# Kernel optimization log

Measured on AMD Instinct MI355X. Metric: run time of the kernel, lower is better.

Reference implementation:

```python
import jax, jax.numpy as jnp
import numpy as np

EPS = 1e-6  # matches nn.CosineSimilarity(eps=1e-6) and the log-denominator eps


def setup_inputs() -> dict:
    key = jax.random.key(0)
    k1, k2 = jax.random.split(key)
    bs, d = 8192, 128
    f = jax.random.normal(k1, (bs, d), dtype=jnp.float32)
    noise = jax.random.normal(k2, (bs, d), dtype=jnp.float32)
    return {"f": f, "noise": noise}


def reference(f, noise):
    bs = f.shape[0]
    cat = jnp.concatenate([noise, f], axis=0)  # [2bs, d]
    # torch CosineSimilarity: x.y / max(||x||*||y||, eps)
    nf = jnp.linalg.norm(f, axis=1)    # [bs]
    nc = jnp.linalg.norm(cat, axis=1)  # [2bs]
    sims = (f @ cat.T) / jnp.maximum(nf[:, None] * nc[None, :], EPS)  # [bs, 2bs]
    m = jnp.exp(sims)
    idx = jnp.arange(bs)
    pos = m[idx, idx]                 # f[i] vs noise[i]
    self_sim = m[idx, idx + bs]       # f[i] vs f[i], excluded from negatives
    neg_sum = m.sum(axis=1) - pos - self_sim
    loss = -jnp.log(pos / (neg_sum + EPS))
    return loss.mean()
```

## Files before the change

### kernel.cpp

```cpp
#include <hip/hip_runtime.h>
#include <hip/hip_bf16.h>
#include <math.h>

#define BS 8192
#define D 128
#define NROWS 16384
#define COLS_PER_BLOCK 512
#define NCHUNK (COLS_PER_BLOCK / 16)
#define NSPLIT (NROWS / COLS_PER_BLOCK)
#define NPART NSPLIT

typedef int i32x4 __attribute__((ext_vector_type(4)));
typedef int i32x8 __attribute__((ext_vector_type(8)));
typedef float f32x4 __attribute__((ext_vector_type(4)));

#define LN2F 0.6931471805599453f
#define STORE_SCALE 19.217958569050494f
#define E8M0_M4 123
#define FMT_FP4 4

#if __has_builtin(__builtin_amdgcn_exp2f)
#define EXP2F(x) __builtin_amdgcn_exp2f(x)
#else
#define EXP2F(x) exp2f(x)
#endif


__global__ __launch_bounds__(256) void nrm_cvt(const float* __restrict__ f,
                                               const float* __restrict__ noise,
                                               char* __restrict__ catF,
                                               unsigned int* __restrict__ cnt) {
  if (blockIdx.x == 0 && threadIdx.x == 0) cnt[0] = 0;
  const int lane = threadIdx.x & 63;
  const int wv = threadIdx.x >> 6;
  const int row = blockIdx.x * 4 + wv;
  const float* src = (row < BS) ? (noise + (size_t)row * D) : (f + (size_t)(row - BS) * D);
  float2 v = ((const float2*)src)[lane];
  float ss = v.x * v.x + v.y * v.y;
#pragma unroll
  for (int m = 1; m <= 32; m <<= 1) ss += __shfl_xor(ss, m, 64);
  const float s = STORE_SCALE / sqrtf(ss);
  auto q4 = [](float x) {
    const float av = fabsf(x);
    int c = (av > 0.25f) + (av > 0.75f) + (av > 1.25f) + (av > 1.75f) +
            (av > 2.5f) + (av > 3.5f) + (av > 5.0f);
    return c | ((x < 0.f) ? 8 : 0);
  };
  const int b = q4(v.x * s) | (q4(v.y * s) << 4);
  const int b1 = __shfl_down(b, 1, 64);
  const int b2 = __shfl_down(b, 2, 64);
  const int b3 = __shfl_down(b, 3, 64);
  if ((lane & 3) == 0) {
    const unsigned word = (unsigned)b | ((unsigned)b1 << 8) |
                          ((unsigned)b2 << 16) | ((unsigned)b3 << 24);
    char* dst = catF + ((size_t)(row >> 4) << 10) + ((lane >> 4) << 8) +
                ((row & 15) << 4) + (lane & 15);
    *(unsigned*)dst = word;
  }
}

__device__ __forceinline__ i32x8 mk8(i32x4 v) {
  i32x8 r = {v[0], v[1], v[2], v[3], 0, 0, 0, 0};
  return r;
}

__global__ __launch_bounds__(256) void infonce_main(
    const char* __restrict__ catF,
    float* __restrict__ ws_neg, float* __restrict__ ws_pos) {
  const int tid = threadIdx.x;
  const int lane = tid & 63;
  const int w = tid >> 6;
  const int l15 = lane & 15, l4 = lane >> 4;
  const int nb = blockIdx.x, mb = blockIdx.y;
  const int growbase = mb * 256 + w * 64;
  const int col0 = nb * COLS_PER_BLOCK;
  const int lbase = l4 * 256 + l15 * 16;

  i32x8 a[4];
  {
    const char* ab = catF + ((size_t)((BS + growbase) >> 4) << 10) + lbase;
#pragma unroll
    for (int rf = 0; rf < 4; rf++) a[rf] = mk8(*(const i32x4*)(ab + rf * 1024));
  }

  f32x4 rs[4];
  const f32x4 z = {0.f, 0.f, 0.f, 0.f};
#pragma unroll
  for (int rf = 0; rf < 4; rf++) rs[rf] = z;

  const char* bl = catF + ((size_t)(col0 >> 4) << 10) + lbase;

  auto ld = [&](int c) { return mk8(*(const i32x4*)(bl + (size_t)c * 1024)); };

  auto domfma = [&](f32x4* acc, const i32x8& b) {
#pragma unroll
    for (int rf = 0; rf < 4; rf++)
      acc[rf] = __builtin_amdgcn_mfma_scale_f32_16x16x128_f8f6f4(
          a[rf], b, z, FMT_FP4, FMT_FP4, 0, E8M0_M4, 0, E8M0_M4);
  };

  auto epi = [&](const f32x4* acc, int c) {
    const int c0 = col0 + c * 16;
    const bool dPos = ((c0 & ~63) == growbase);
    const bool dSelf = (((c0 - BS) & ~63) == growbase);
    if (!dPos && !dSelf) {
#pragma unroll
      for (int rf = 0; rf < 4; rf++) {
        f32x4 e;
#pragma unroll
        for (int r = 0; r < 4; r++) e[r] = EXP2F(acc[rf][r]);
        rs[rf] += e;
      }
    } else {
#pragma unroll
      for (int rf = 0; rf < 4; rf++)
#pragma unroll
        for (int r = 0; r < 4; r++) {
          const int grow = growbase + rf * 16 + l4 * 4 + r;
          const int gcol = c0 + l15;
          const float v = acc[rf][r];
          const bool ex = dPos ? (gcol == grow) : (gcol == grow + BS);
          if (dPos && gcol == grow) ws_pos[grow] = v;
          rs[rf][r] += ex ? 0.f : EXP2F(v);
        }
    }
  };

  i32x8 bb[4];
  bb[0] = ld(0);
  bb[1] = ld(1);

  f32x4 accA[4], accB[4];
  domfma(accA, bb[0]);
  bb[2] = ld(2);
  domfma(accB, bb[1]);
  bb[3] = ld(3);

#pragma unroll
  for (int ph = 0; ph < 15; ++ph) {
    const int c = 2 * ph;
    __builtin_amdgcn_sched_barrier(0);
    epi(accA, c);
    if (c + 4 < NCHUNK) bb[(c + 4) & 3] = ld(c + 4);
    domfma(accA, bb[(c + 2) & 3]);
    __builtin_amdgcn_sched_barrier(0);
    epi(accB, c + 1);
    if (c + 5 < NCHUNK) bb[(c + 5) & 3] = ld(c + 5);
    domfma(accB, bb[(c + 3) & 3]);
  }
  __builtin_amdgcn_sched_barrier(0);
  epi(accA, NCHUNK - 2);
  epi(accB, NCHUNK - 1);

  float rowsum[16];
#pragma unroll
  for (int rf = 0; rf < 4; rf++)
#pragma unroll
    for (int r = 0; r < 4; r++) {
      float v = rs[rf][r];
      v += __shfl_xor(v, 1, 64);
      v += __shfl_xor(v, 2, 64);
      v += __shfl_xor(v, 4, 64);
      v += __shfl_xor(v, 8, 64);
      rowsum[rf * 4 + r] = v;
    }
  if (l15 == 0) {
    float* dst = ws_neg + (size_t)nb * BS + growbase;
#pragma unroll
    for (int rf = 0; rf < 4; rf++)
#pragma unroll
      for (int r = 0; r < 4; r++) dst[rf * 16 + l4 * 4 + r] = rowsum[rf * 4 + r];
  }
}

__global__ __launch_bounds__(256) void finalize(const float* __restrict__ ws_neg,
                                                const float* __restrict__ ws_pos,
                                                float* __restrict__ partial,
                                                unsigned int* __restrict__ cnt,
                                                float* __restrict__ out) {
  __shared__ float red[4];
  __shared__ int flag;
  const int tid = threadIdx.x;
  const int lane = tid & 63;
  const int w = tid >> 6;
  const int row = blockIdx.x * 256 + tid;
  float neg = 0.f;
#pragma unroll
  for (int p = 0; p < NPART; p++) neg += ws_neg[(size_t)p * BS + row];
  float local = logf(neg + 1e-6f) - ws_pos[row] * LN2F;
#pragma unroll
  for (int m = 1; m <= 32; m <<= 1) local += __shfl_xor(local, m, 64);
  if (lane == 0) red[w] = local;
  __syncthreads();
  if (tid == 0) {
    partial[blockIdx.x] = red[0] + red[1] + red[2] + red[3];
    __threadfence();
    flag = (atomicAdd(cnt, 1u) == (unsigned)(BS / 256 - 1));
  }
  __syncthreads();
  if (!flag) return;
  __threadfence();
  if (tid < 64) {
    float v = (tid < 32) ? partial[tid] : 0.f;
#pragma unroll
    for (int m = 1; m <= 32; m <<= 1) v += __shfl_xor(v, m, 64);
    if (tid == 0) out[0] = v * (1.f / BS);
  }
}

extern "C" void kernel_launch(void* const* d_in, const int* in_sizes, int n_in,
                              void* d_out, int out_size, void* d_ws, size_t ws_size,
                              hipStream_t stream) {
  const float* f = (const float*)d_in[0];
  const float* noise = (const float*)d_in[1];
  char* ws = (char*)d_ws;
  char* catF = ws;
  float* ws_pos = (float*)(ws + (size_t)NROWS * 64);
  float* ws_neg = ws_pos + BS;
  float* partial = ws_neg + (size_t)NPART * BS;
  unsigned int* cnt = (unsigned int*)(partial + 32);

  nrm_cvt<<<NROWS / 4, 256, 0, stream>>>(f, noise, catF, cnt);
  dim3 grid(NSPLIT, BS / 256);
  infonce_main<<<grid, 256, 0, stream>>>(catF, ws_neg, ws_pos);
  finalize<<<BS / 256, 256, 0, stream>>>(ws_neg, ws_pos, partial, cnt, (float*)d_out);
}
```

Before: 36.11 us.

## Exploit symmetry of f·fᵀ block to halve self-similarity MFMA and exp work

Splits the work into noise-column jobs and upper-triangular f×f tile jobs. Each off-diagonal f×f tile adds its exp values to both row sums and column partial sums, so the symmetric half is never computed. Diagonal tiles mask the lower triangle, which also drops the self-similarity term. The aim is to cut MFMA and exp work on the f×f half by about half. In exchange the kernel adds shared-memory column reductions, a triangular index mapping, and a heavier finalize pass that reads more partial buffers.

```diff
diff --git a/kernel.cpp b/kernel.cpp
--- a/kernel.cpp
+++ b/kernel.cpp
@@ -5,10 +5,9 @@
 #define BS 8192
 #define D 128
 #define NROWS 16384
-#define COLS_PER_BLOCK 512
-#define NCHUNK (COLS_PER_BLOCK / 16)
-#define NSPLIT (NROWS / COLS_PER_BLOCK)
-#define NPART NSPLIT
+#define NJOBS_N 512
+#define NJOBS_F 528
+#define NJOBS (NJOBS_N + NJOBS_F)
 
 typedef int i32x4 __attribute__((ext_vector_type(4)));
 typedef int i32x8 __attribute__((ext_vector_type(8)));
@@ -66,114 +65,212 @@
 
 __global__ __launch_bounds__(256) void infonce_main(
     const char* __restrict__ catF,
-    float* __restrict__ ws_neg, float* __restrict__ ws_pos) {
+    float* __restrict__ wsN, float* __restrict__ rowF,
+    float* __restrict__ colP, float* __restrict__ ws_pos) {
+  __shared__ float cls[4][256];
   const int tid = threadIdx.x;
   const int lane = tid & 63;
   const int w = tid >> 6;
   const int l15 = lane & 15, l4 = lane >> 4;
-  const int nb = blockIdx.x, mb = blockIdx.y;
-  const int growbase = mb * 256 + w * 64;
-  const int col0 = nb * COLS_PER_BLOCK;
+  const int jid = blockIdx.x;
+  const f32x4 z = {0.f, 0.f, 0.f, 0.f};
+
+  f32x4 rs[4];
+#pragma unroll
+  for (int rf = 0; rf < 4; rf++) rs[rf] = z;
   const int lbase = l4 * 256 + l15 * 16;
 
-  i32x8 a[4];
-  {
-    const char* ab = catF + ((size_t)((BS + growbase) >> 4) << 10) + lbase;
-#pragma unroll
-    for (int rf = 0; rf < 4; rf++) a[rf] = mk8(*(const i32x4*)(ab + rf * 1024));
+  if (jid < NJOBS_N) {
+    const int mb = jid >> 4, nb = jid & 15;
+    const int growbase = mb * 256 + w * 64;
+    const int col0 = nb * 512;
+
+    i32x8 a[4];
+    {
+      const char* ab = catF + ((size_t)((BS + growbase) >> 4) << 10) + lbase;
+#pragma unroll
+      for (int rf = 0; rf < 4; rf++) a[rf] = mk8(*(const i32x4*)(ab + rf * 1024));
+    }
+    const char* bl = catF + ((size_t)(col0 >> 4) << 10) + lbase;
+    auto ld = [&](int c) { return mk8(*(const i32x4*)(bl + (size_t)c * 1024)); };
+    auto domfma = [&](f32x4* acc, const i32x8& b) {
+#pragma unroll
+      for (int rf = 0; rf < 4; rf++)
+        acc[rf] = __builtin_amdgcn_mfma_scale_f32_16x16x128_f8f6f4(
+            a[rf], b, z, FMT_FP4, FMT_FP4, 0, E8M0_M4, 0, E8M0_M4);
+    };
+    auto epi = [&](const f32x4* acc, int c) {
+      const int c0 = col0 + c * 16;
+      if ((c0 & ~63) != growbase) {
+#pragma unroll
+        for (int rf = 0; rf < 4; rf++) {
+          f32x4 e;
+#pragma unroll
+          for (int r = 0; r < 4; r++) e[r] = EXP2F(acc[rf][r]);
+          rs[rf] += e;
+        }
+      } else {
+#pragma unroll
+        for (int rf = 0; rf < 4; rf++)
+#pragma unroll
+          for (int r = 0; r < 4; r++) {
+            const int grow = growbase + rf * 16 + l4 * 4 + r;
+            const int gcol = c0 + l15;
+            const float v = acc[rf][r];
+            const bool ex = (gcol == grow);
+            if (ex) ws_pos[grow] = v;
+            rs[rf][r] += ex ? 0.f : EXP2F(v);
+          }
+      }
+    };
+
+    i32x8 bb[4];
+    bb[0] = ld(0);
+    bb[1] = ld(1);
+    f32x4 accA[4], accB[4];
+    domfma(accA, bb[0]);
+    bb[2] = ld(2);
+    domfma(accB, bb[1]);
+    bb[3] = ld(3);
+#pragma unroll
+    for (int ph = 0; ph < 15; ++ph) {
+      const int c = 2 * ph;
+      __builtin_amdgcn_sched_barrier(0);
+      epi(accA, c);
+      if (c + 4 < 32) bb[(c + 4) & 3] = ld(c + 4);
+      domfma(accA, bb[(c + 2) & 3]);
+      __builtin_amdgcn_sched_barrier(0);
+      epi(accB, c + 1);
+      if (c + 5 < 32) bb[(c + 5) & 3] = ld(c + 5);
+      domfma(accB, bb[(c + 3) & 3]);
+    }
+    __builtin_amdgcn_sched_barrier(0);
+    epi(accA, 30);
+    epi(accB, 31);
+
+    float rowsum[16];
+#pragma unroll
+    for (int rf = 0; rf < 4; rf++)
+#pragma unroll
+      for (int r = 0; r < 4; r++) {
+        float v = rs[rf][r];
+        v += __shfl_xor(v, 1, 64);
+        v += __shfl_xor(v, 2, 64);
+        v += __shfl_xor(v, 4, 64);
+        v += __shfl_xor(v, 8, 64);
+        rowsum[rf * 4 + r] = v;
+      }
+    if (l15 == 0) {
+      float* dst = wsN + (size_t)nb * BS + growbase;
+#pragma unroll
+      for (int rf = 0; rf < 4; rf++)
+#pragma unroll
+        for (int r = 0; r < 4; r++) dst[rf * 16 + l4 * 4 + r] = rowsum[rf * 4 + r];
+    }
+  } else {
+    const int t = jid - NJOBS_N;
+    int g = (int)((65.0f - sqrtf(4225.0f - 8.0f * (float)t)) * 0.5f);
+    while ((g + 1) * (65 - (g + 1)) / 2 <= t) ++g;
+    while (g * (65 - g) / 2 > t) --g;
+    const int h = g + (t - g * (65 - g) / 2);
+    const bool diag = (h == g);
+    const int growbase = g * 256 + w * 64;
+    const int colf0 = h * 256;
+
+    i32x8 a[4];
+    {
+      const char* ab = catF + ((size_t)((BS + growbase) >> 4) << 10) + lbase;
+#pragma unroll
+      for (int rf = 0; rf < 4; rf++) a[rf] = mk8(*(const i32x4*)(ab + rf * 1024));
+    }
+    const char* bl = catF + ((size_t)((BS + colf0) >> 4) << 10) + lbase;
+    auto ld = [&](int c) { return mk8(*(const i32x4*)(bl + (size_t)c * 1024)); };
+    auto domfma = [&](f32x4* acc, const i32x8& b) {
+#pragma unroll
+      for (int rf = 0; rf < 4; rf++)
+        acc[rf] = __builtin_amdgcn_mfma_scale_f32_16x16x128_f8f6f4(
+            a[rf], b, z, FMT_FP4, FMT_FP4, 0, E8M0_M4, 0, E8M0_M4);
+    };
+    auto epi = [&](const f32x4* acc, int c) {
+      float csum = 0.f;
+      if (!diag) {
+#pragma unroll
+        for (int rf = 0; rf < 4; rf++)
+#pragma unroll
+          for (int r = 0; r < 4; r++) {
+            const float e = EXP2F(acc[rf][r]);
+            rs[rf][r] += e;
+            csum += e;
+          }
+      } else {
+        const int gcol = colf0 + c * 16 + l15;
+#pragma unroll
+        for (int rf = 0; rf < 4; rf++)
+#pragma unroll
+          for (int r = 0; r < 4; r++) {
+            const int grow = growbase + rf * 16 + l4 * 4 + r;
+            const float e = (gcol > grow) ? EXP2F(acc[rf][r]) : 0.f;
+            rs[rf][r] += e;
+            csum += e;
+          }
+      }
+      csum += __shfl_xor(csum, 16, 64);
+      csum += __shfl_xor(csum, 32, 64);
+      if (l4 == 0) cls[w][c * 16 + l15] = csum;
+    };
+
+    i32x8 bb[4];
+    bb[0] = ld(0);
+    bb[1] = ld(1);
+    f32x4 accA[4], accB[4];
+    domfma(accA, bb[0]);
+    bb[2] = ld(2);
+    domfma(accB, bb[1]);
+    bb[3] = ld(3);
+#pragma unroll
+    for (int ph = 0; ph < 7; ++ph) {
+      const int c = 2 * ph;
+      __builtin_amdgcn_sched_barrier(0);
+      epi(accA, c);
+      if (c + 4 < 16) bb[(c + 4) & 3] = ld(c + 4);
+      domfma(accA, bb[(c + 2) & 3]);
+      __builtin_amdgcn_sched_barrier(0);
+      epi(accB, c + 1);
+      if (c + 5 < 16) bb[(c + 5) & 3] = ld(c + 5);
+      domfma(accB, bb[(c + 3) & 3]);
+    }
+    __builtin_amdgcn_sched_barrier(0);
+    epi(accA, 14);
+    epi(accB, 15);
+
+    float rowsum[16];
+#pragma unroll
+    for (int rf = 0; rf < 4; rf++)
+#pragma unroll
+      for (int r = 0; r < 4; r++) {
+        float v = rs[rf][r];
+        v += __shfl_xor(v, 1, 64);
+        v += __shfl_xor(v, 2, 64);
+        v += __shfl_xor(v, 4, 64);
+        v += __shfl_xor(v, 8, 64);
+        rowsum[rf * 4 + r] = v;
+      }
+    if (l15 == 0) {
+      float* dst = rowF + (size_t)h * BS + growbase;
+#pragma unroll
+      for (int rf = 0; rf < 4; rf++)
+#pragma unroll
+        for (int r = 0; r < 4; r++) dst[rf * 16 + l4 * 4 + r] = rowsum[rf * 4 + r];
+    }
+    __syncthreads();
+    colP[(size_t)g * BS + colf0 + tid] =
+        cls[0][tid] + cls[1][tid] + cls[2][tid] + cls[3][tid];
   }
-
-  f32x4 rs[4];
-  const f32x4 z = {0.f, 0.f, 0.f, 0.f};
-#pragma unroll
-  for (int rf = 0; rf < 4; rf++) rs[rf] = z;
-
-  const char* bl = catF + ((size_t)(col0 >> 4) << 10) + lbase;
-
-  auto ld = [&](int c) { return mk8(*(const i32x4*)(bl + (size_t)c * 1024)); };
-
-  auto domfma = [&](f32x4* acc, const i32x8& b) {
-#pragma unroll
-    for (int rf = 0; rf < 4; rf++)
-      acc[rf] = __builtin_amdgcn_mfma_scale_f32_16x16x128_f8f6f4(
-          a[rf], b, z, FMT_FP4, FMT_FP4, 0, E8M0_M4, 0, E8M0_M4);
-  };
-
-  auto epi = [&](const f32x4* acc, int c) {
-    const int c0 = col0 + c * 16;
-    const bool dPos = ((c0 & ~63) == growbase);
-    const bool dSelf = (((c0 - BS) & ~63) == growbase);
-    if (!dPos && !dSelf) {
-#pragma unroll
-      for (int rf = 0; rf < 4; rf++) {
-        f32x4 e;
-#pragma unroll
-        for (int r = 0; r < 4; r++) e[r] = EXP2F(acc[rf][r]);
-        rs[rf] += e;
-      }
-    } else {
-#pragma unroll
-      for (int rf = 0; rf < 4; rf++)
-#pragma unroll
-        for (int r = 0; r < 4; r++) {
-          const int grow = growbase + rf * 16 + l4 * 4 + r;
-          const int gcol = c0 + l15;
-          const float v = acc[rf][r];
-          const bool ex = dPos ? (gcol == grow) : (gcol == grow + BS);
-          if (dPos && gcol == grow) ws_pos[grow] = v;
-          rs[rf][r] += ex ? 0.f : EXP2F(v);
-        }
-    }
-  };
-
-  i32x8 bb[4];
-  bb[0] = ld(0);
-  bb[1] = ld(1);
-
-  f32x4 accA[4], accB[4];
-  domfma(accA, bb[0]);
-  bb[2] = ld(2);
-  domfma(accB, bb[1]);
-  bb[3] = ld(3);
-
-#pragma unroll
-  for (int ph = 0; ph < 15; ++ph) {
-    const int c = 2 * ph;
-    __builtin_amdgcn_sched_barrier(0);
-    epi(accA, c);
-    if (c + 4 < NCHUNK) bb[(c + 4) & 3] = ld(c + 4);
-    domfma(accA, bb[(c + 2) & 3]);
-    __builtin_amdgcn_sched_barrier(0);
-    epi(accB, c + 1);
-    if (c + 5 < NCHUNK) bb[(c + 5) & 3] = ld(c + 5);
-    domfma(accB, bb[(c + 3) & 3]);
-  }
-  __builtin_amdgcn_sched_barrier(0);
-  epi(accA, NCHUNK - 2);
-  epi(accB, NCHUNK - 1);
-
-  float rowsum[16];
-#pragma unroll
-  for (int rf = 0; rf < 4; rf++)
-#pragma unroll
-    for (int r = 0; r < 4; r++) {
-      float v = rs[rf][r];
-      v += __shfl_xor(v, 1, 64);
-      v += __shfl_xor(v, 2, 64);
-      v += __shfl_xor(v, 4, 64);
-      v += __shfl_xor(v, 8, 64);
-      rowsum[rf * 4 + r] = v;
-    }
-  if (l15 == 0) {
-    float* dst = ws_neg + (size_t)nb * BS + growbase;
-#pragma unroll
-    for (int rf = 0; rf < 4; rf++)
-#pragma unroll
-      for (int r = 0; r < 4; r++) dst[rf * 16 + l4 * 4 + r] = rowsum[rf * 4 + r];
-  }
-}
-
-__global__ __launch_bounds__(256) void finalize(const float* __restrict__ ws_neg,
+}
+
+__global__ __launch_bounds__(256) void finalize(const float* __restrict__ wsN,
+                                                const float* __restrict__ rowF,
+                                                const float* __restrict__ colP,
                                                 const float* __restrict__ ws_pos,
                                                 float* __restrict__ partial,
                                                 unsigned int* __restrict__ cnt,
@@ -184,9 +281,12 @@
   const int lane = tid & 63;
   const int w = tid >> 6;
   const int row = blockIdx.x * 256 + tid;
+  const int gr = row >> 8;
   float neg = 0.f;
 #pragma unroll
-  for (int p = 0; p < NPART; p++) neg += ws_neg[(size_t)p * BS + row];
+  for (int p = 0; p < 16; p++) neg += wsN[(size_t)p * BS + row];
+  for (int h = gr; h < 32; h++) neg += rowF[(size_t)h * BS + row];
+  for (int g = 0; g <= gr; g++) neg += colP[(size_t)g * BS + row];
   float local = logf(neg + 1e-6f) - ws_pos[row] * LN2F;
 #pragma unroll
   for (int m = 1; m <= 32; m <<= 1) local += __shfl_xor(local, m, 64);
@@ -216,12 +316,14 @@
   char* ws = (char*)d_ws;
   char* catF = ws;
   float* ws_pos = (float*)(ws + (size_t)NROWS * 64);
-  float* ws_neg = ws_pos + BS;
-  float* partial = ws_neg + (size_t)NPART * BS;
+  float* wsN = ws_pos + BS;
+  float* rowF = wsN + (size_t)16 * BS;
+  float* colP = rowF + (size_t)32 * BS;
+  float* partial = colP + (size_t)32 * BS;
   unsigned int* cnt = (unsigned int*)(partial + 32);
 
   nrm_cvt<<<NROWS / 4, 256, 0, stream>>>(f, noise, catF, cnt);
-  dim3 grid(NSPLIT, BS / 256);
-  infonce_main<<<grid, 256, 0, stream>>>(catF, ws_neg, ws_pos);
-  finalize<<<BS / 256, 256, 0, stream>>>(ws_neg, ws_pos, partial, cnt, (float*)d_out);
-}
+  infonce_main<<<NJOBS, 256, 0, stream>>>(catF, wsN, rowF, colP, ws_pos);
+  finalize<<<BS / 256, 256, 0, stream>>>(wsN, rowF, colP, ws_pos, partial, cnt,
+                                         (float*)d_out);
+}
```

Result: slower. 55.43 us (+53.5%).
